# Kernel tuning notes

Measured on AMD Instinct MI355X. Metric: run time of the kernel, lower is better.

## Reference

```python
import jax, jax.numpy as jnp
import numpy as np

NUM_HEADS = 16
GROUP_NUM = 4
HIDDEN = 1024
HEAD_DIM = HIDDEN // NUM_HEADS
EPS = 1e-5


def layernorm(x, g, b):
    mu = jnp.mean(x, axis=-1, keepdims=True)
    var = jnp.var(x, axis=-1, keepdims=True)
    return (x - mu) * jax.lax.rsqrt(var + EPS) * g + b


def setup_inputs() -> dict:
    key = jax.random.key(0)
    ks = jax.random.split(key, 12)
    s = 0.02
    return {
        "hidden_state": jax.random.normal(ks[0], (2, 2048, HIDDEN), jnp.float32),
        "wq": jax.random.normal(ks[1], (HIDDEN, HIDDEN), jnp.float32) * s,
        "bq": jnp.zeros((HIDDEN,), jnp.float32),
        "wk": jax.random.normal(ks[2], (GROUP_NUM * HEAD_DIM, HIDDEN), jnp.float32) * s,
        "bk": jnp.zeros((GROUP_NUM * HEAD_DIM,), jnp.float32),
        "wv": jax.random.normal(ks[3], (GROUP_NUM * HEAD_DIM, HIDDEN), jnp.float32) * s,
        "bv": jnp.zeros((GROUP_NUM * HEAD_DIM,), jnp.float32),
        "wo": jax.random.normal(ks[4], (HIDDEN, HIDDEN), jnp.float32) * s,
        "bo": jnp.zeros((HIDDEN,), jnp.float32),
        "ln_g": jnp.ones((HIDDEN,), jnp.float32),
        "ln_b": jnp.zeros((HIDDEN,), jnp.float32),
        "w1": jax.random.normal(ks[5], (HIDDEN, HIDDEN), jnp.float32) * s,
        "b1": jnp.zeros((HIDDEN,), jnp.float32),
        "w2": jax.random.normal(ks[6], (HIDDEN, HIDDEN), jnp.float32) * s,
        "b2": jnp.zeros((HIDDEN,), jnp.float32),
        "fln_g": jnp.ones((HIDDEN,), jnp.float32),
        "fln_b": jnp.zeros((HIDDEN,), jnp.float32),
    }


def reference(hidden_state, wq, bq, wk, bk, wv, bv, wo, bo, ln_g, ln_b,
              w1, b1, w2, b2, fln_g, fln_b):
    B, S, H = hidden_state.shape
    hpg = NUM_HEADS // GROUP_NUM  # heads per KV group

    q = hidden_state @ wq.T + bq  # [B,S,H]
    k = hidden_state @ wk.T + bk  # [B,S,G*D]
    v = hidden_state @ wv.T + bv

    q = q.reshape(B, S, NUM_HEADS, HEAD_DIM).transpose(0, 2, 1, 3)      # [B,Hh,S,D]
    k = k.reshape(B, S, GROUP_NUM, HEAD_DIM).transpose(0, 2, 1, 3)      # [B,G,S,D]
    v = v.reshape(B, S, GROUP_NUM, HEAD_DIM).transpose(0, 2, 1, 3)
    # expand KV groups to full head count (consecutive repeat, matching torch expand+reshape)
    k = jnp.repeat(k, hpg, axis=1)  # [B,Hh,S,D]
    v = jnp.repeat(v, hpg, axis=1)

    scale = 1.0 / jnp.sqrt(jnp.float32(HEAD_DIM))
    scores = jnp.einsum('bhsd,bhtd->bhst', q, k) * scale  # [B,Hh,S,S]
    probs = jax.nn.softmax(scores, axis=-1)
    attn = jnp.einsum('bhst,bhtd->bhsd', probs, v)  # [B,Hh,S,D]

    # Faithful to source: transpose(-1,-2) then raw flat view to [B, S, Hh*D]
    attn = jnp.swapaxes(attn, -1, -2).reshape(B, -1, HEAD_DIM * NUM_HEADS)

    out = layernorm(hidden_state + attn @ wo.T + bo, ln_g, ln_b)
    ffn = out @ w1.T + b1
    ffn = jax.nn.relu(ffn) @ w2.T + b2
    return layernorm(out + ffn, fln_g, fln_b)
```

## Files before the change

### kernel.cpp

```cpp
#include <hip/hip_runtime.h>
#include <math.h>

#define HIDDEN 1024
#define SEQ 2048

typedef __attribute__((ext_vector_type(8))) short short8;
typedef __attribute__((ext_vector_type(4))) float f32x4;

__device__ __forceinline__ unsigned short f2bf(float x) {
  union { float f; unsigned u; } c; c.f = x;
  unsigned r = c.u + 0x7FFFu + ((c.u >> 16) & 1u);
  return (unsigned short)(r >> 16);
}
__device__ __forceinline__ float bf2f(unsigned short h) {
  union { unsigned u; float f; } c; c.u = ((unsigned)h) << 16;
  return c.f;
}

__device__ __forceinline__ void async_copy16(const void* g, void* l) {
  __builtin_amdgcn_global_load_lds(
      (const __attribute__((address_space(1))) unsigned int*)g,
      (__attribute__((address_space(3))) unsigned int*)l, 16, 0, 0);
}

__global__ __launch_bounds__(256) void cvt_all(
    const float* __restrict__ hs, const float* __restrict__ wq,
    const float* __restrict__ wk, const float* __restrict__ wv,
    const float* __restrict__ wo, const float* __restrict__ w1,
    const float* __restrict__ w2,
    unsigned short* __restrict__ hsb, unsigned short* __restrict__ wqb,
    unsigned short* __restrict__ wkb, unsigned short* __restrict__ wvb,
    unsigned short* __restrict__ wob, unsigned short* __restrict__ w1b,
    unsigned short* __restrict__ w2b)
{
  const int i = blockIdx.x * 256 + threadIdx.x;
  const float* src; unsigned short* dst; int off;
  if (i < 1048576)      { src = hs; dst = hsb; off = i; }
  else if (i < 1310720) { src = wq; dst = wqb; off = i - 1048576; }
  else if (i < 1376256) { src = wk; dst = wkb; off = i - 1310720; }
  else if (i < 1441792) { src = wv; dst = wvb; off = i - 1376256; }
  else if (i < 1703936) { src = wo; dst = wob; off = i - 1441792; }
  else if (i < 1966080) { src = w1; dst = w1b; off = i - 1703936; }
  else                  { src = w2; dst = w2b; off = i - 1966080; }
  float4 v = ((const float4*)src)[off];
  ushort4 o;
  o.x = f2bf(v.x); o.y = f2bf(v.y); o.z = f2bf(v.z); o.w = f2bf(v.w);
  ((ushort4*)dst)[off] = o;
}

template<bool RELU>
__global__ __launch_bounds__(256) void gemm_mfma(
    const unsigned short* __restrict__ A, const unsigned short* __restrict__ W,
    const float* __restrict__ bias, unsigned short* __restrict__ C,
    int M, int N, int K)
{
  __shared__ unsigned short As[64 * 64];
  __shared__ unsigned short Bs[64 * 64];
  const int tid = threadIdx.x;
  const int lane = tid & 63, wave = tid >> 6;
  const int ln = lane & 15, quad = lane >> 4;
  const int wm = (wave >> 1) * 32, wn = (wave & 1) * 32;
  const int m0 = blockIdx.y * 64, n0 = blockIdx.x * 64;

  f32x4 acc[2][2];
#pragma unroll
  for (int i = 0; i < 2; ++i)
#pragma unroll
    for (int j = 0; j < 2; ++j) acc[i][j] = (f32x4){0.f, 0.f, 0.f, 0.f};

  for (int k0 = 0; k0 < K; k0 += 64) {
#pragma unroll
    for (int it = 0; it < 2; ++it) {
      const int c = (wave * 2 + it) * 64 + lane;
      const int row = c >> 3, gc = (c & 7) ^ (row & 7);
      async_copy16(A + (size_t)(m0 + row) * K + k0 + gc * 8,
                   &As[(wave * 2 + it) * 512]);
      async_copy16(W + (size_t)(n0 + row) * K + k0 + gc * 8,
                   &Bs[(wave * 2 + it) * 512]);
    }
    __syncthreads();

    short8 af[2][2], bfr[2][2];
#pragma unroll
    for (int i = 0; i < 2; ++i) {
      const int row = wm + i * 16 + ln;
#pragma unroll
      for (int f = 0; f < 2; ++f) {
        const int ch = row * 8 + ((f * 4 + quad) ^ (row & 7));
        af[i][f] = *(const short8*)&As[ch * 8];
      }
    }
#pragma unroll
    for (int j = 0; j < 2; ++j) {
      const int row = wn + j * 16 + ln;
#pragma unroll
      for (int f = 0; f < 2; ++f) {
        const int ch = row * 8 + ((f * 4 + quad) ^ (row & 7));
        bfr[j][f] = *(const short8*)&Bs[ch * 8];
      }
    }
#pragma unroll
    for (int i = 0; i < 2; ++i)
#pragma unroll
      for (int j = 0; j < 2; ++j) {
        acc[i][j] = __builtin_amdgcn_mfma_f32_16x16x32_bf16(af[i][0], bfr[j][0], acc[i][j], 0, 0, 0);
        acc[i][j] = __builtin_amdgcn_mfma_f32_16x16x32_bf16(af[i][1], bfr[j][1], acc[i][j], 0, 0, 0);
      }
    __syncthreads();
  }

#pragma unroll
  for (int j = 0; j < 2; ++j) {
    const int n = n0 + wn + j * 16 + ln;
    const float bv = bias[n];
#pragma unroll
    for (int i = 0; i < 2; ++i) {
#pragma unroll
      for (int rr = 0; rr < 4; ++rr) {
        const int m = m0 + wm + i * 16 + quad * 4 + rr;
        float v = acc[i][j][rr] + bv;
        if (RELU) v = fmaxf(v, 0.f);
        C[(size_t)m * N + n] = f2bf(v);
      }
    }
  }
}

__global__ __launch_bounds__(256) void gemm_qkv(
    const unsigned short* __restrict__ A,
    const unsigned short* __restrict__ Wq, const unsigned short* __restrict__ Wk,
    const unsigned short* __restrict__ Wv,
    const float* __restrict__ bq, const float* __restrict__ bk,
    const float* __restrict__ bv,
    unsigned short* __restrict__ Qo, unsigned short* __restrict__ Ko,
    unsigned short* __restrict__ Vt)
{
  __shared__ unsigned short As[64 * 64];
  __shared__ unsigned short Bs[128 * 64];
  const int bx = blockIdx.x;
  int mode, nw0;
  const unsigned short* W;
  const float* bias;
  if (bx < 8)       { mode = 0; W = Wq; bias = bq; nw0 = bx * 128; }
  else if (bx < 10) { mode = 1; W = Wk; bias = bk; nw0 = (bx - 8) * 128; }
  else              { mode = 2; W = Wv; bias = bv; nw0 = (bx - 10) * 128; }

  const int tid = threadIdx.x;
  const int lane = tid & 63, wave = tid >> 6;
  const int ln = lane & 15, quad = lane >> 4;
  const int wm = (wave >> 1) * 32, wn = (wave & 1) * 64;
  const int m0 = blockIdx.y * 64;
  const int K = 1024;

  f32x4 acc[2][4];
#pragma unroll
  for (int i = 0; i < 2; ++i)
#pragma unroll
    for (int j = 0; j < 4; ++j) acc[i][j] = (f32x4){0.f, 0.f, 0.f, 0.f};

  for (int k0 = 0; k0 < K; k0 += 64) {
#pragma unroll
    for (int it = 0; it < 2; ++it) {
      const int c = (wave * 2 + it) * 64 + lane;
      const int row = c >> 3, gc = (c & 7) ^ (row & 7);
      async_copy16(A + (size_t)(m0 + row) * K + k0 + gc * 8,
                   &As[(wave * 2 + it) * 512]);
    }
#pragma unroll
    for (int it = 0; it < 4; ++it) {
      const int c = (wave * 4 + it) * 64 + lane;
      const int row = c >> 3, gc = (c & 7) ^ (row & 7);
      async_copy16(W + (size_t)(nw0 + row) * K + k0 + gc * 8,
                   &Bs[(wave * 4 + it) * 512]);
    }
    __syncthreads();

    short8 af[2][2], bfr[4][2];
#pragma unroll
    for (int i = 0; i < 2; ++i) {
      const int row = wm + i * 16 + ln;
#pragma unroll
      for (int f = 0; f < 2; ++f) {
        const int ch = row * 8 + ((f * 4 + quad) ^ (row & 7));
        af[i][f] = *(const short8*)&As[ch * 8];
      }
    }
#pragma unroll
    for (int j = 0; j < 4; ++j) {
      const int row = wn + j * 16 + ln;
#pragma unroll
      for (int f = 0; f < 2; ++f) {
        const int ch = row * 8 + ((f * 4 + quad) ^ (row & 7));
        bfr[j][f] = *(const short8*)&Bs[ch * 8];
      }
    }
#pragma unroll
    for (int i = 0; i < 2; ++i)
#pragma unroll
      for (int j = 0; j < 4; ++j) {
        acc[i][j] = __builtin_amdgcn_mfma_f32_16x16x32_bf16(af[i][0], bfr[j][0], acc[i][j], 0, 0, 0);
        acc[i][j] = __builtin_amdgcn_mfma_f32_16x16x32_bf16(af[i][1], bfr[j][1], acc[i][j], 0, 0, 0);
      }
    __syncthreads();
  }

#pragma unroll
  for (int j = 0; j < 4; ++j) {
    const int nl = nw0 + wn + j * 16 + ln;
    const float bvv = bias[nl];
#pragma unroll
    for (int i = 0; i < 2; ++i) {
#pragma unroll
      for (int rr = 0; rr < 4; ++rr) {
        const int m = m0 + wm + i * 16 + quad * 4 + rr;
        const float v = acc[i][j][rr] + bvv;
        if (mode == 0) {
          Qo[(size_t)m * 1024 + nl] = f2bf(v);
        } else if (mode == 1) {
          Ko[(size_t)m * 256 + nl] = f2bf(v);
        } else {
          const int b = m >> 11, s = m & 2047;
          Vt[((size_t)b * 256 + nl) * SEQ + s] = f2bf(v);
        }
      }
    }
  }
}

__global__ __launch_bounds__(256) void attn_mfma(
    const unsigned short* __restrict__ Q, const unsigned short* __restrict__ Kb,
    const unsigned short* __restrict__ Vt, unsigned short* __restrict__ O)
{
  __shared__ unsigned short Ks[64 * 64];
  __shared__ unsigned short Vs[64 * 64];
  __shared__ unsigned short Ps[4 * 16 * 64];

  const int bid = blockIdx.x;
  const int qblk = bid & 31, h = (bid >> 5) & 15, b = bid >> 9, g = h >> 2;
  const int tid = threadIdx.x, lane = tid & 63, wave = tid >> 6;
  const int ln = lane & 15, quad = lane >> 4, q8 = quad * 8;
  const int s0 = qblk * 64;
  const float qscale = 0.125f * 1.44269504f;

  const int ln7 = ln & 7;
  const int x0 = (quad ^ ln7) * 8;
  const int x1 = ((4 + quad) ^ ln7) * 8;
  const int pswz = 2 * ln7;
  const int pbase = wave * 1024 + ln * 64;
  int pwr[4], prd[2];
#pragma unroll
  for (int jn = 0; jn < 4; ++jn) pwr[jn] = pbase + (((jn * 4 + quad) ^ pswz) << 2);
#pragma unroll
  for (int F = 0; F < 2; ++F)   prd[F] = pbase + (((8 * F + 2 * quad) ^ pswz) << 2);

  short8 ones;
#pragma unroll
  for (int e = 0; e < 8; ++e) ones[e] = (short)0x3F80;

  short8 qf0, qf1;
  {
    const unsigned short* qsrc =
        Q + ((size_t)(b * SEQ + s0 + wave * 16 + ln)) * 1024 + h * 64 + q8;
    qf0 = *(const short8*)qsrc;
    qf1 = *(const short8*)(qsrc + 32);
#pragma unroll
    for (int e = 0; e < 8; ++e) {
      qf0[e] = (short)f2bf(bf2f((unsigned short)qf0[e]) * qscale);
      qf1[e] = (short)f2bf(bf2f((unsigned short)qf1[e]) * qscale);
    }
  }

  const int srow = lane >> 3;
  const int sgcc = (lane & 7) ^ srow;

  f32x4 of[4];
  f32x4 ls = (f32x4){0.f, 0.f, 0.f, 0.f};
#pragma unroll
  for (int jd = 0; jd < 4; ++jd) of[jd] = (f32x4){0.f, 0.f, 0.f, 0.f};

  for (int t0 = 0; t0 < SEQ; t0 += 64) {
    {
#pragma unroll
      for (int it = 0; it < 2; ++it) {
        const int row = wave * 16 + it * 8 + srow;
        async_copy16(Kb + (size_t)(b * SEQ + t0 + row) * 256 + g * 64 + sgcc * 8,
                     &Ks[(wave * 2 + it) * 512]);
        async_copy16(Vt + (size_t)(b * 256 + g * 64 + row) * SEQ + t0 + sgcc * 8,
                     &Vs[(wave * 2 + it) * 512]);
      }
    }
    __syncthreads();

    f32x4 sc[4];
#pragma unroll
    for (int jn = 0; jn < 4; ++jn) {
      const int krow = (jn * 16 + ln) * 64;
      const short8 kf0 = *(const short8*)&Ks[krow + x0];
      const short8 kf1 = *(const short8*)&Ks[krow + x1];
      f32x4 z = (f32x4){0.f, 0.f, 0.f, 0.f};
      z = __builtin_amdgcn_mfma_f32_16x16x32_bf16(kf0, qf0, z, 0, 0, 0);
      z = __builtin_amdgcn_mfma_f32_16x16x32_bf16(kf1, qf1, z, 0, 0, 0);
      sc[jn] = z;
    }

#pragma unroll
    for (int jn = 0; jn < 4; ++jn) {
      union { float f; unsigned u; } c0, c1, c2, c3;
      c0.f = exp2f(sc[jn][0]);
      c1.f = exp2f(sc[jn][1]);
      c2.f = exp2f(sc[jn][2]);
      c3.f = exp2f(sc[jn][3]);
      uint2 pk;
      pk.x = __builtin_amdgcn_perm(c1.u, c0.u, 0x07060302u);
      pk.y = __builtin_amdgcn_perm(c3.u, c2.u, 0x07060302u);
      *(uint2*)&Ps[pwr[jn]] = pk;
    }

    const short8 pf0 = *(const short8*)&Ps[prd[0]];
    const short8 pf1 = *(const short8*)&Ps[prd[1]];
    ls = __builtin_amdgcn_mfma_f32_16x16x32_bf16(pf0, ones, ls, 0, 0, 0);
    ls = __builtin_amdgcn_mfma_f32_16x16x32_bf16(pf1, ones, ls, 0, 0, 0);
#pragma unroll
    for (int jd = 0; jd < 4; ++jd) {
      const int vrow = (jd * 16 + ln) * 64;
      const short8 vf0 = *(const short8*)&Vs[vrow + x0];
      const short8 vf1 = *(const short8*)&Vs[vrow + x1];
      of[jd] = __builtin_amdgcn_mfma_f32_16x16x32_bf16(pf0, vf0, of[jd], 0, 0, 0);
      of[jd] = __builtin_amdgcn_mfma_f32_16x16x32_bf16(pf1, vf1, of[jd], 0, 0, 0);
    }
    __syncthreads();
  }

  float inv[4];
#pragma unroll
  for (int r = 0; r < 4; ++r) inv[r] = 1.0f / ls[r];

  const int sbase = s0 + wave * 16 + quad * 4;
#pragma unroll
  for (int jd = 0; jd < 4; ++jd) {
    const int d = jd * 16 + ln;
    ushort4 ov;
    ov.x = f2bf(of[jd][0] * inv[0]);
    ov.y = f2bf(of[jd][1] * inv[1]);
    ov.z = f2bf(of[jd][2] * inv[2]);
    ov.w = f2bf(of[jd][3] * inv[3]);
    *(ushort4*)&O[((size_t)b * 1024 + h * 64 + d) * SEQ + sbase] = ov;
  }
}

__device__ __forceinline__ void ln_core(float x[4], const float* gam, const float* bet,
                                        int tid, float out[4]) {
  float s1 = x[0] + x[1] + x[2] + x[3];
  float s2 = x[0] * x[0] + x[1] * x[1] + x[2] * x[2] + x[3] * x[3];
#pragma unroll
  for (int off = 1; off < 64; off <<= 1) {
    s1 += __shfl_xor(s1, off);
    s2 += __shfl_xor(s2, off);
  }
  __shared__ float r1[4], r2[4];
  const int wave = tid >> 6;
  if ((tid & 63) == 0) { r1[wave] = s1; r2[wave] = s2; }
  __syncthreads();
  s1 = r1[0] + r1[1] + r1[2] + r1[3];
  s2 = r2[0] + r2[1] + r2[2] + r2[3];
  const float mu  = s1 * (1.0f / HIDDEN);
  const float var = s2 * (1.0f / HIDDEN) - mu * mu;
  const float inv = rsqrtf(var + 1e-5f);
  float4 gv = *(const float4*)&gam[tid * 4];
  float4 bv = *(const float4*)&bet[tid * 4];
  out[0] = (x[0] - mu) * inv * gv.x + bv.x;
  out[1] = (x[1] - mu) * inv * gv.y + bv.y;
  out[2] = (x[2] - mu) * inv * gv.z + bv.z;
  out[3] = (x[3] - mu) * inv * gv.w + bv.w;
}

__global__ __launch_bounds__(256) void resid_ln1(
    const float* __restrict__ X, const unsigned short* __restrict__ Y,
    const float* __restrict__ gam, const float* __restrict__ bet,
    unsigned short* __restrict__ outb)
{
  const int row = blockIdx.x, tid = threadIdx.x;
  const size_t base = (size_t)row * HIDDEN + tid * 4;
  float4 a = *(const float4*)&X[base];
  ushort4 yv = *(const ushort4*)&Y[base];
  float x[4] = {a.x + bf2f(yv.x), a.y + bf2f(yv.y), a.z + bf2f(yv.z), a.w + bf2f(yv.w)};
  float o[4];
  ln_core(x, gam, bet, tid, o);
  ushort4 ov;
  ov.x = f2bf(o[0]); ov.y = f2bf(o[1]); ov.z = f2bf(o[2]); ov.w = f2bf(o[3]);
  *(ushort4*)&outb[base] = ov;
}

__global__ __launch_bounds__(256) void resid_ln2(
    const unsigned short* __restrict__ X, const unsigned short* __restrict__ Y,
    const float* __restrict__ gam, const float* __restrict__ bet,
    float* __restrict__ out)
{
  const int row = blockIdx.x, tid = threadIdx.x;
  const size_t base = (size_t)row * HIDDEN + tid * 4;
  ushort4 xv = *(const ushort4*)&X[base];
  ushort4 yv = *(const ushort4*)&Y[base];
  float x[4] = {bf2f(xv.x) + bf2f(yv.x), bf2f(xv.y) + bf2f(yv.y),
                bf2f(xv.z) + bf2f(yv.z), bf2f(xv.w) + bf2f(yv.w)};
  float o[4];
  ln_core(x, gam, bet, tid, o);
  float4 ov; ov.x = o[0]; ov.y = o[1]; ov.z = o[2]; ov.w = o[3];
  *(float4*)&out[base] = ov;
}

extern "C" void kernel_launch(void* const* d_in, const int* in_sizes, int n_in,
                              void* d_out, int out_size, void* d_ws, size_t ws_size,
                              hipStream_t stream)
{
  (void)in_sizes; (void)n_in; (void)out_size; (void)ws_size;
  const float* hs  = (const float*)d_in[0];
  const float* wq  = (const float*)d_in[1];
  const float* bq  = (const float*)d_in[2];
  const float* wk  = (const float*)d_in[3];
  const float* bk  = (const float*)d_in[4];
  const float* wv  = (const float*)d_in[5];
  const float* bvp = (const float*)d_in[6];
  const float* wo  = (const float*)d_in[7];
  const float* bo  = (const float*)d_in[8];
  const float* lng = (const float*)d_in[9];
  const float* lnb = (const float*)d_in[10];
  const float* w1  = (const float*)d_in[11];
  const float* b1  = (const float*)d_in[12];
  const float* w2  = (const float*)d_in[13];
  const float* b2  = (const float*)d_in[14];
  const float* flg = (const float*)d_in[15];
  const float* flb = (const float*)d_in[16];
  float* out = (float*)d_out;

  unsigned short* w = (unsigned short*)d_ws;
  unsigned short* wqb = w;
  unsigned short* wkb = w + 1048576;
  unsigned short* wvb = w + 1310720;
  unsigned short* wob = w + 1572864;
  unsigned short* w1b = w + 2621440;
  unsigned short* w2b = w + 3670016;
  unsigned short* hsb = w + 4718592;
  unsigned short* qb  = w + 8912896;
  unsigned short* kb  = w + 13107200;
  unsigned short* vt  = w + 14155776;
  unsigned short* att = w + 15204352;
  unsigned short* f1b = hsb;
  unsigned short* yb  = qb;
  unsigned short* obb = att;
  unsigned short* f2b = qb;

  dim3 blk(256);
  cvt_all<<<dim3(8704), blk, 0, stream>>>(hs, wq, wk, wv, wo, w1, w2,
                                          hsb, wqb, wkb, wvb, wob, w1b, w2b);

  gemm_qkv<<<dim3(12, 64), blk, 0, stream>>>(hsb, wqb, wkb, wvb, bq, bk, bvp,
                                             qb, kb, vt);
  attn_mfma<<<dim3(1024), blk, 0, stream>>>(qb, kb, vt, att);
  gemm_mfma<false><<<dim3(16, 64), blk, 0, stream>>>(att, wob, bo, yb, 4096, 1024, 1024);
  resid_ln1<<<dim3(4096), blk, 0, stream>>>(hs, yb, lng, lnb, obb);
  gemm_mfma<true><<<dim3(16, 64), blk, 0, stream>>>(obb, w1b, b1, f1b, 4096, 1024, 1024);
  gemm_mfma<false><<<dim3(16, 64), blk, 0, stream>>>(f1b, w2b, b2, f2b, 4096, 1024, 1024);
  resid_ln2<<<dim3(4096), blk, 0, stream>>>(obb, f2b, flg, flb, out);
}
```

Baseline: 258.5 us.

## Double-buffer K/V tiles and process two query groups per wave in attention

The attention kernel now prefetches the next K/V tile into a second LDS buffer with async copies while computing on the current one, using explicit vmcnt waits and raw barriers in place of a full sync before compute. Each wave now handles 32 query rows (two 16-row groups), so every K/V fragment read from LDS feeds twice as many MFMAs, and the grid is halved to 512 blocks. This aims to hide global load latency and cut LDS traffic per unit of compute. The cost is more registers and LDS per block and fewer blocks, which may lower occupancy on 256 CUs.

```diff
diff --git a/kernel.cpp b/kernel.cpp
--- a/kernel.cpp
+++ b/kernel.cpp
@@ -231,22 +231,22 @@
     const unsigned short* __restrict__ Q, const unsigned short* __restrict__ Kb,
     const unsigned short* __restrict__ Vt, unsigned short* __restrict__ O)
 {
-  __shared__ unsigned short Ks[64 * 64];
-  __shared__ unsigned short Vs[64 * 64];
-  __shared__ unsigned short Ps[4 * 16 * 64];
+  __shared__ unsigned short Ks[2][64 * 64];
+  __shared__ unsigned short Vs[2][64 * 64];
+  __shared__ unsigned short Ps[4 * 2 * 16 * 64];
 
   const int bid = blockIdx.x;
-  const int qblk = bid & 31, h = (bid >> 5) & 15, b = bid >> 9, g = h >> 2;
+  const int qblk = bid & 15, h = (bid >> 4) & 15, b = bid >> 8, g = h >> 2;
   const int tid = threadIdx.x, lane = tid & 63, wave = tid >> 6;
   const int ln = lane & 15, quad = lane >> 4, q8 = quad * 8;
-  const int s0 = qblk * 64;
+  const int s0 = qblk * 128;
   const float qscale = 0.125f * 1.44269504f;
 
   const int ln7 = ln & 7;
   const int x0 = (quad ^ ln7) * 8;
   const int x1 = ((4 + quad) ^ ln7) * 8;
   const int pswz = 2 * ln7;
-  const int pbase = wave * 1024 + ln * 64;
+  const int pbase = wave * 2048 + ln * 64;
   int pwr[4], prd[2];
 #pragma unroll
   for (int jn = 0; jn < 4; ++jn) pwr[jn] = pbase + (((jn * 4 + quad) ^ pswz) << 2);
@@ -257,94 +257,127 @@
 #pragma unroll
   for (int e = 0; e < 8; ++e) ones[e] = (short)0x3F80;
 
-  short8 qf0, qf1;
-  {
+  short8 qf[2][2];
+#pragma unroll
+  for (int qg = 0; qg < 2; ++qg) {
     const unsigned short* qsrc =
-        Q + ((size_t)(b * SEQ + s0 + wave * 16 + ln)) * 1024 + h * 64 + q8;
-    qf0 = *(const short8*)qsrc;
-    qf1 = *(const short8*)(qsrc + 32);
+        Q + ((size_t)(b * SEQ + s0 + wave * 32 + qg * 16 + ln)) * 1024 + h * 64 + q8;
+    qf[qg][0] = *(const short8*)qsrc;
+    qf[qg][1] = *(const short8*)(qsrc + 32);
 #pragma unroll
     for (int e = 0; e < 8; ++e) {
-      qf0[e] = (short)f2bf(bf2f((unsigned short)qf0[e]) * qscale);
-      qf1[e] = (short)f2bf(bf2f((unsigned short)qf1[e]) * qscale);
+      qf[qg][0][e] = (short)f2bf(bf2f((unsigned short)qf[qg][0][e]) * qscale);
+      qf[qg][1][e] = (short)f2bf(bf2f((unsigned short)qf[qg][1][e]) * qscale);
     }
   }
 
   const int srow = lane >> 3;
   const int sgcc = (lane & 7) ^ srow;
 
-  f32x4 of[4];
-  f32x4 ls = (f32x4){0.f, 0.f, 0.f, 0.f};
-#pragma unroll
-  for (int jd = 0; jd < 4; ++jd) of[jd] = (f32x4){0.f, 0.f, 0.f, 0.f};
-
-  for (int t0 = 0; t0 < SEQ; t0 += 64) {
-    {
-#pragma unroll
-      for (int it = 0; it < 2; ++it) {
-        const int row = wave * 16 + it * 8 + srow;
-        async_copy16(Kb + (size_t)(b * SEQ + t0 + row) * 256 + g * 64 + sgcc * 8,
-                     &Ks[(wave * 2 + it) * 512]);
-        async_copy16(Vt + (size_t)(b * 256 + g * 64 + row) * SEQ + t0 + sgcc * 8,
-                     &Vs[(wave * 2 + it) * 512]);
-      }
-    }
-    __syncthreads();
-
-    f32x4 sc[4];
+  auto stage = [&](int t0, int p) {
+#pragma unroll
+    for (int it = 0; it < 2; ++it) {
+      const int row = wave * 16 + it * 8 + srow;
+      async_copy16(Kb + (size_t)(b * SEQ + t0 + row) * 256 + g * 64 + sgcc * 8,
+                   &Ks[p][(wave * 2 + it) * 512]);
+      async_copy16(Vt + (size_t)(b * 256 + g * 64 + row) * SEQ + t0 + sgcc * 8,
+                   &Vs[p][(wave * 2 + it) * 512]);
+    }
+  };
+
+  f32x4 of[2][4];
+  f32x4 ls[2];
+#pragma unroll
+  for (int qg = 0; qg < 2; ++qg) {
+    ls[qg] = (f32x4){0.f, 0.f, 0.f, 0.f};
+#pragma unroll
+    for (int jd = 0; jd < 4; ++jd) of[qg][jd] = (f32x4){0.f, 0.f, 0.f, 0.f};
+  }
+
+  stage(0, 0);
+
+  for (int t = 0; t < 32; ++t) {
+    const int p = t & 1;
+    if (t < 31) {
+      stage((t + 1) * 64, p ^ 1);
+      asm volatile("s_waitcnt vmcnt(4)" ::: "memory");
+    } else {
+      asm volatile("s_waitcnt vmcnt(0)" ::: "memory");
+    }
+    __builtin_amdgcn_s_barrier();
+    asm volatile("" ::: "memory");
+
+    f32x4 sc[2][4];
 #pragma unroll
     for (int jn = 0; jn < 4; ++jn) {
       const int krow = (jn * 16 + ln) * 64;
-      const short8 kf0 = *(const short8*)&Ks[krow + x0];
-      const short8 kf1 = *(const short8*)&Ks[krow + x1];
-      f32x4 z = (f32x4){0.f, 0.f, 0.f, 0.f};
-      z = __builtin_amdgcn_mfma_f32_16x16x32_bf16(kf0, qf0, z, 0, 0, 0);
-      z = __builtin_amdgcn_mfma_f32_16x16x32_bf16(kf1, qf1, z, 0, 0, 0);
-      sc[jn] = z;
-    }
-
-#pragma unroll
-    for (int jn = 0; jn < 4; ++jn) {
-      union { float f; unsigned u; } c0, c1, c2, c3;
-      c0.f = exp2f(sc[jn][0]);
-      c1.f = exp2f(sc[jn][1]);
-      c2.f = exp2f(sc[jn][2]);
-      c3.f = exp2f(sc[jn][3]);
-      uint2 pk;
-      pk.x = __builtin_amdgcn_perm(c1.u, c0.u, 0x07060302u);
-      pk.y = __builtin_amdgcn_perm(c3.u, c2.u, 0x07060302u);
-      *(uint2*)&Ps[pwr[jn]] = pk;
-    }
-
-    const short8 pf0 = *(const short8*)&Ps[prd[0]];
-    const short8 pf1 = *(const short8*)&Ps[prd[1]];
-    ls = __builtin_amdgcn_mfma_f32_16x16x32_bf16(pf0, ones, ls, 0, 0, 0);
-    ls = __builtin_amdgcn_mfma_f32_16x16x32_bf16(pf1, ones, ls, 0, 0, 0);
+      const short8 kf0 = *(const short8*)&Ks[p][krow + x0];
+      const short8 kf1 = *(const short8*)&Ks[p][krow + x1];
+#pragma unroll
+      for (int qg = 0; qg < 2; ++qg) {
+        f32x4 z = (f32x4){0.f, 0.f, 0.f, 0.f};
+        z = __builtin_amdgcn_mfma_f32_16x16x32_bf16(kf0, qf[qg][0], z, 0, 0, 0);
+        z = __builtin_amdgcn_mfma_f32_16x16x32_bf16(kf1, qf[qg][1], z, 0, 0, 0);
+        sc[qg][jn] = z;
+      }
+    }
+
+#pragma unroll
+    for (int qg = 0; qg < 2; ++qg)
+#pragma unroll
+      for (int jn = 0; jn < 4; ++jn) {
+        union { float f; unsigned u; } c0, c1, c2, c3;
+        c0.f = exp2f(sc[qg][jn][0]);
+        c1.f = exp2f(sc[qg][jn][1]);
+        c2.f = exp2f(sc[qg][jn][2]);
+        c3.f = exp2f(sc[qg][jn][3]);
+        uint2 pk;
+        pk.x = __builtin_amdgcn_perm(c1.u, c0.u, 0x07060302u);
+        pk.y = __builtin_amdgcn_perm(c3.u, c2.u, 0x07060302u);
+        *(uint2*)&Ps[qg * 1024 + pwr[jn]] = pk;
+      }
+
+    short8 pf[2][2];
+#pragma unroll
+    for (int qg = 0; qg < 2; ++qg) {
+      pf[qg][0] = *(const short8*)&Ps[qg * 1024 + prd[0]];
+      pf[qg][1] = *(const short8*)&Ps[qg * 1024 + prd[1]];
+      ls[qg] = __builtin_amdgcn_mfma_f32_16x16x32_bf16(pf[qg][0], ones, ls[qg], 0, 0, 0);
+      ls[qg] = __builtin_amdgcn_mfma_f32_16x16x32_bf16(pf[qg][1], ones, ls[qg], 0, 0, 0);
+    }
 #pragma unroll
     for (int jd = 0; jd < 4; ++jd) {
       const int vrow = (jd * 16 + ln) * 64;
-      const short8 vf0 = *(const short8*)&Vs[vrow + x0];
-      const short8 vf1 = *(const short8*)&Vs[vrow + x1];
-      of[jd] = __builtin_amdgcn_mfma_f32_16x16x32_bf16(pf0, vf0, of[jd], 0, 0, 0);
-      of[jd] = __builtin_amdgcn_mfma_f32_16x16x32_bf16(pf1, vf1, of[jd], 0, 0, 0);
-    }
-    __syncthreads();
-  }
-
-  float inv[4];
-#pragma unroll
-  for (int r = 0; r < 4; ++r) inv[r] = 1.0f / ls[r];
-
-  const int sbase = s0 + wave * 16 + quad * 4;
-#pragma unroll
-  for (int jd = 0; jd < 4; ++jd) {
-    const int d = jd * 16 + ln;
-    ushort4 ov;
-    ov.x = f2bf(of[jd][0] * inv[0]);
-    ov.y = f2bf(of[jd][1] * inv[1]);
-    ov.z = f2bf(of[jd][2] * inv[2]);
-    ov.w = f2bf(of[jd][3] * inv[3]);
-    *(ushort4*)&O[((size_t)b * 1024 + h * 64 + d) * SEQ + sbase] = ov;
+      const short8 vf0 = *(const short8*)&Vs[p][vrow + x0];
+      const short8 vf1 = *(const short8*)&Vs[p][vrow + x1];
+#pragma unroll
+      for (int qg = 0; qg < 2; ++qg) {
+        of[qg][jd] = __builtin_amdgcn_mfma_f32_16x16x32_bf16(pf[qg][0], vf0, of[qg][jd], 0, 0, 0);
+        of[qg][jd] = __builtin_amdgcn_mfma_f32_16x16x32_bf16(pf[qg][1], vf1, of[qg][jd], 0, 0, 0);
+      }
+    }
+
+    asm volatile("" ::: "memory");
+    __builtin_amdgcn_s_barrier();
+    asm volatile("" ::: "memory");
+  }
+
+#pragma unroll
+  for (int qg = 0; qg < 2; ++qg) {
+    float inv[4];
+#pragma unroll
+    for (int r = 0; r < 4; ++r) inv[r] = 1.0f / ls[qg][r];
+    const int sbase = s0 + wave * 32 + qg * 16 + quad * 4;
+#pragma unroll
+    for (int jd = 0; jd < 4; ++jd) {
+      const int d = jd * 16 + ln;
+      ushort4 ov;
+      ov.x = f2bf(of[qg][jd][0] * inv[0]);
+      ov.y = f2bf(of[qg][jd][1] * inv[1]);
+      ov.z = f2bf(of[qg][jd][2] * inv[2]);
+      ov.w = f2bf(of[qg][jd][3] * inv[3]);
+      *(ushort4*)&O[((size_t)b * 1024 + h * 64 + d) * SEQ + sbase] = ov;
+    }
   }
 }
 
@@ -455,7 +488,7 @@
 
   gemm_qkv<<<dim3(12, 64), blk, 0, stream>>>(hsb, wqb, wkb, wvb, bq, bk, bvp,
                                              qb, kb, vt);
-  attn_mfma<<<dim3(1024), blk, 0, stream>>>(qb, kb, vt, att);
+  attn_mfma<<<dim3(512), blk, 0, stream>>>(qb, kb, vt, att);
   gemm_mfma<false><<<dim3(16, 64), blk, 0, stream>>>(att, wob, bo, yb, 4096, 1024, 1024);
   resid_ln1<<<dim3(4096), blk, 0, stream>>>(hs, yb, lng, lnb, obb);
   gemm_mfma<true><<<dim3(16, 64), blk, 0, stream>>>(obb, w1b, b1, f1b, 4096, 1024, 1024);
```

After: 254.9 us. No clear change (-1.4%).
